# Kernel optimization log

Hardware: AMD Instinct MI355X
Metric: run time of the kernel (lower is better)

## Reference

```python
import jax, jax.numpy as jnp
import numpy as np

T, B, D = 160, 640, 40      # time-major frames, batch (N_spk*M_utt), log-mel dim
H, P, L = 768, 256, 3       # nb_hidden, nb_proj, nb_layers


def setup_inputs() -> dict:
    key = jax.random.key(0)
    ks = jax.random.split(key, 1 + 3 * L)
    inp = {"x": jax.random.normal(ks[0], (T, B, D), jnp.float32)}
    din = D
    for l in range(L):
        gs = np.float32(np.sqrt(2.0 / (din + P + 4 * H)))  # glorot-ish scale
        inp[f"W{l}"] = jax.random.normal(ks[1 + 3 * l], (din + P, 4 * H), jnp.float32) * gs
        inp[f"b{l}"] = jnp.zeros((4 * H,), jnp.float32)
        ps = np.float32(np.sqrt(2.0 / (H + P)))
        inp[f"Wp{l}"] = jax.random.normal(ks[3 + 3 * l], (H, P), jnp.float32) * ps
        din = P
    return inp


def lstmp_layer(x, W, b, Wp):
    # x: [T, B, d_in] time-major. TF LSTMCell with num_proj: state h has dim P,
    # gate order (i, j, f, o), forget_bias = 1.0.
    bsz = x.shape[1]
    c0 = jnp.zeros((bsz, H), x.dtype)
    h0 = jnp.zeros((bsz, P), x.dtype)

    def step(carry, xt):
        c, h = carry
        z = jnp.concatenate([xt, h], axis=-1) @ W + b            # [B, 4H]
        i, j, f, o = jnp.split(z, 4, axis=-1)
        c = jax.nn.sigmoid(f + 1.0) * c + jax.nn.sigmoid(i) * jnp.tanh(j)
        h = (jax.nn.sigmoid(o) * jnp.tanh(c)) @ Wp               # projection -> [B, P]
        return (c, h), h

    _, ys = jax.lax.scan(step, (c0, h0), x)                      # ys: [T, B, P]
    return ys


def reference(x, W0, b0, Wp0, W1, b1, Wp1, W2, b2, Wp2):
    h = lstmp_layer(x, W0, b0, Wp0)
    h = lstmp_layer(h, W1, b1, Wp1)
    h = lstmp_layer(h, W2, b2, Wp2)
    emb = h[-1]                                                  # last timestep: [B, P]
    return emb / (jnp.linalg.norm(emb, axis=-1, keepdims=True) + 1e-6)
```

## Files before the change

### kernel.cpp

```cpp
#include <hip/hip_runtime.h>
#include <hip/hip_bf16.h>

typedef __attribute__((ext_vector_type(4))) float f32x4;
typedef __attribute__((ext_vector_type(8))) short s16x8;

#define DEVFN static __device__ __forceinline__

#define TT  160
#define BB  640
#define DD  40
#define HH  768
#define PP  256
#define G4H 3072

#define NWG   192
#define NTHR  256

#define KH  256
#define KX0 64

#define STW1 328
#define STW2 520
#define STP  776
#define LDS_ELEMS 66560

#define XP_BYTES   (TT*BB*64*2)
#define HR_BYTES   (3*4*BB*PP*2)
#define SB_BYTES   (3*BB*HH*2)
#define XP_OFF     0
#define HR_OFF     (XP_OFF + XP_BYTES)
#define SB_OFF     (HR_OFF + HR_BYTES)
#define SYNC_OFF   (SB_OFF + SB_BYTES)
#define SYNC_BYTES 4096

DEVFN float sigm(float v)  { return __fdividef(1.f, 1.f + __expf(-v)); }
DEVFN float tanh_(float v) { return 2.f * __fdividef(1.f, 1.f + __expf(-2.f * v)) - 1.f; }
DEVFN f32x4 f4zero() { f32x4 v; v[0]=0.f; v[1]=0.f; v[2]=0.f; v[3]=0.f; return v; }

DEVFN void gst_b16(__hip_bfloat16* p, __hip_bfloat16 v) {
  unsigned short u = __builtin_bit_cast(unsigned short, v);
  asm volatile("global_store_short %0, %1, off sc0 sc1" :: "v"(p), "v"(u));
}

DEVFN unsigned ld_cc(const unsigned* p) {
  unsigned v;
  asm volatile("global_load_dword %0, %1, off sc0 sc1\n\ts_waitcnt vmcnt(0)"
               : "=v"(v) : "v"(p) : "memory");
  return v;
}
DEVFN void st_cc(unsigned* p, unsigned v) {
  asm volatile("global_store_dword %0, %1, off sc0 sc1" :: "v"(p), "v"(v) : "memory");
}
DEVFN void ld3_cc(const unsigned* p0, const unsigned* p1, const unsigned* p2,
                  unsigned& a, unsigned& b, unsigned& c) {
  asm volatile("global_load_dword %0, %3, off sc0 sc1\n\t"
               "global_load_dword %1, %4, off sc0 sc1\n\t"
               "global_load_dword %2, %5, off sc0 sc1\n\t"
               "s_waitcnt vmcnt(0)"
               : "=&v"(a), "=&v"(b), "=&v"(c)
               : "v"(p0), "v"(p1), "v"(p2) : "memory");
}

DEVFN void fence_acq() { __builtin_amdgcn_fence(__ATOMIC_ACQUIRE, "agent"); }

#define SFLAG(s,l,g) ((s) + 256 + ((l)*48+(g))*4)
#define PFLAG(s,l,p) ((s) + 832 + ((l)*16+(p))*4)

DEVFN void init_barrier(unsigned* sync, int bid, int tid) {
  __syncthreads();
  if (tid == 0) st_cc(sync + bid, 1u);
  if (tid < 64) {
    unsigned a, b, c;
    for (;;) {
      ld3_cc(sync + tid, sync + 64 + tid, sync + 128 + tid, a, b, c);
      if (__all((a >= 1u) & (b >= 1u) & (c >= 1u))) break;
    }
    fence_acq();
  }
  __syncthreads();
}

DEVFN void wait_flags(const unsigned* base, int nf, int thr, int tid) {
  if (thr <= 0) return;
  if (tid < 64) {
    const unsigned* p = base + tid * 4;
    for (;;) {
      int v = (tid < nf) ? (int)ld_cc(p) : 0x7fffffff;
      if (__all(v >= thr)) break;
    }
    fence_acq();
  }
  __syncthreads();
}

DEVFN void wait_proj(const unsigned* sf_l, const unsigned* sf_lp1, int has2,
                     int thr1, int thr2, int tid) {
  if (tid < 64) {
    const unsigned* p1 = sf_l + tid * 4;
    const unsigned* p2 = sf_lp1 + tid * 4;
    for (;;) {
      int v1 = (tid < 48) ? (int)ld_cc(p1) : 0x7fffffff;
      int v2 = (has2 && tid < 48 && thr2 > 0) ? (int)ld_cc(p2) : 0x7fffffff;
      if (__all((v1 >= thr1) & (v2 >= thr2))) break;
    }
    fence_acq();
  }
  __syncthreads();
}

DEVFN void set_flag(unsigned* p, unsigned v, int tid) {
  __syncthreads();
  if (tid == 0) st_cc(p, v);
}

__global__ __launch_bounds__(NTHR, 1)
void lstmp_persistent(const float* __restrict__ xin,
                      const float* __restrict__ W0, const float* __restrict__ b0, const float* __restrict__ Wp0,
                      const float* __restrict__ W1, const float* __restrict__ b1, const float* __restrict__ Wp1,
                      const float* __restrict__ W2, const float* __restrict__ b2, const float* __restrict__ Wp2,
                      float* __restrict__ outp, unsigned char* __restrict__ ws)
{
  __shared__ __align__(16) __hip_bfloat16 lds[LDS_ELEMS];

  const int bid  = blockIdx.x;
  const int tid  = threadIdx.x;
  const int lane = tid & 63;
  const int wave = tid >> 6;
  const int q    = lane >> 4;
  const int c16  = lane & 15;

  __hip_bfloat16* Xp = (__hip_bfloat16*)(ws + XP_OFF);
  __hip_bfloat16* Hr = (__hip_bfloat16*)(ws + HR_OFF);
  __hip_bfloat16* Sb = (__hip_bfloat16*)(ws + SB_OFF);
  unsigned* sync     = (unsigned*)(ws + SYNC_OFF);

  const int xcd  = bid & 7;
  const int slot = bid >> 3;
  const bool isGate = (xcd < 6);
  int l = 0, bc = 0, hg = 0, mt = 0, nt = 0;
  if (isGate) { l = xcd >> 1; bc = xcd & 1; hg = slot; }
  else        { l = slot >> 3; int r = slot & 7; mt = (xcd - 6) * 2 + (r >> 2); nt = r & 3; }

  const int KX  = (l == 0) ? KX0 : 256;
  const int KT  = KX + KH;
  const int STW = (l == 0) ? STW1 : STW2;

  const float* Wl  = (l == 0) ? W0  : ((l == 1) ? W1  : W2);
  const float* bl  = (l == 0) ? b0  : ((l == 1) ? b1  : b2);
  const float* Wpl = (l == 0) ? Wp0 : ((l == 1) ? Wp1 : Wp2);

  for (int e = bid * NTHR + tid; e < TT * BB * 64; e += NWG * NTHR) {
    int k  = e & 63;
    int tb = e >> 6;
    float v = (k < DD) ? xin[(size_t)tb * DD + k] : 0.f;
    gst_b16(&Xp[e], __float2bfloat16(v));
  }

  if (isGate) {
    for (int idx = tid; idx < 128 * KT; idx += NTHR) {
      int kk = idx >> 7;
      int nn = idx & 127;
      int col = (nn >> 5) * HH + hg * 32 + (nn & 31);
      float v;
      if (l == 0) {
        v = (kk < DD) ? Wl[(size_t)kk * G4H + col]
                      : ((kk < KX0) ? 0.f : Wl[(size_t)(kk - 24) * G4H + col]);
      } else {
        v = Wl[(size_t)kk * G4H + col];
      }
      lds[nn * STW + kk] = __float2bfloat16(v);
    }
  } else {
    for (int idx = tid; idx < 64 * HH; idx += NTHR) {
      int kk = idx >> 6;
      int nn = idx & 63;
      lds[nn * STP + kk] = __float2bfloat16(Wpl[(size_t)kk * PP + nt * 64 + nn]);
    }
  }

  init_barrier(sync, bid, tid);

  if (isGate) {
    const int gid = bc * 24 + hg;
    unsigned* myflag = SFLAG(sync, l, gid);
    const unsigned* pf_own = PFLAG(sync, l, 0);
    const unsigned* pf_prv = (l > 0) ? PFLAG(sync, l - 1, 0) : PFLAG(sync, l, 0);

    const int wmg = wave >> 1, wng = wave & 1;
    const int m0g = bc * 320 + wmg * 160;
    const int hcl = wng * 16 + c16;
    float biasv[4];
#pragma unroll
    for (int g = 0; g < 4; ++g) biasv[g] = bl[g * HH + hg * 32 + hcl];

    f32x4 acc[10][4];
    float cst[10][4];
#pragma unroll
    for (int mi = 0; mi < 10; ++mi)
#pragma unroll
      for (int g = 0; g < 4; ++g) { acc[mi][g] = f4zero(); cst[mi][g] = 0.f; }

    auto gate_gemm = [&](const __hip_bfloat16* A, int lda, int kbase, int klen) {
      s16x8 avA[5], avB[5];
#pragma unroll
      for (int mi = 0; mi < 5; ++mi)
        avA[mi] = *(const s16x8*)(A + (size_t)(m0g + mi * 16 + c16) * lda + 8 * q);
#pragma unroll 1
      for (int ks = 0; ks < klen; ks += 32) {
#pragma unroll
        for (int mi = 0; mi < 5; ++mi)
          avB[mi] = *(const s16x8*)(A + (size_t)(m0g + (5 + mi) * 16 + c16) * lda + ks + 8 * q);
        s16x8 bv[4];
#pragma unroll
        for (int g = 0; g < 4; ++g)
          bv[g] = *(const s16x8*)(lds + (g * 32 + hcl) * STW + kbase + ks + 8 * q);
#pragma unroll
        for (int mi = 0; mi < 5; ++mi)
#pragma unroll
          for (int g = 0; g < 4; ++g)
            acc[mi][g] = __builtin_amdgcn_mfma_f32_16x16x32_bf16(avA[mi], bv[g], acc[mi][g], 0, 0, 0);
        if (ks + 32 < klen) {
#pragma unroll
          for (int mi = 0; mi < 5; ++mi)
            avA[mi] = *(const s16x8*)(A + (size_t)(m0g + mi * 16 + c16) * lda + ks + 32 + 8 * q);
        }
#pragma unroll
        for (int mi = 0; mi < 5; ++mi)
#pragma unroll
          for (int g = 0; g < 4; ++g)
            acc[5 + mi][g] = __builtin_amdgcn_mfma_f32_16x16x32_bf16(avB[mi], bv[g], acc[5 + mi][g], 0, 0, 0);
      }
    };

    auto gate_update = [&]() {
      __hip_bfloat16* S = Sb + (size_t)l * BB * HH;
#pragma unroll
      for (int mi = 0; mi < 10; ++mi) {
#pragma unroll
        for (int r = 0; r < 4; ++r) {
          float iv = acc[mi][0][r] + biasv[0];
          float jv = acc[mi][1][r] + biasv[1];
          float fv = acc[mi][2][r] + biasv[2];
          float ov = acc[mi][3][r] + biasv[3];
          float c  = sigm(fv + 1.f) * cst[mi][r] + sigm(iv) * tanh_(jv);
          cst[mi][r] = c;
          float sv = sigm(ov) * tanh_(c);
          gst_b16(&S[(size_t)(m0g + mi * 16 + q * 4 + r) * HH + hg * 32 + hcl],
                  __float2bfloat16(sv));
        }
#pragma unroll
        for (int g = 0; g < 4; ++g) acc[mi][g] = f4zero();
      }
    };

    if (l == 0) gate_gemm(Xp, 64, 0, KX0);
    else {
      wait_flags(pf_prv, 16, 1, tid);
      gate_gemm(Hr + ((size_t)(l - 1) * 4 + 1) * BB * PP, PP, 0, 256);
    }

    for (int t = 0; t < TT; ++t) {
      wait_flags(pf_own, 16, t, tid);
      gate_gemm(Hr + ((size_t)l * 4 + ((unsigned)t & 3)) * BB * PP, PP, KX, KH);
      gate_update();
      set_flag(myflag, (unsigned)(t + 1), tid);
      if (t + 1 < TT) {
        if (l == 0) gate_gemm(Xp + (size_t)(t + 1) * BB * 64, 64, 0, KX0);
        else {
          wait_flags(pf_prv, 16, t + 2, tid);
          gate_gemm(Hr + ((size_t)(l - 1) * 4 + ((unsigned)(t + 2) & 3)) * BB * PP, PP, 0, 256);
        }
      }
    }
  } else {
    const int pid = mt * 4 + nt;
    unsigned* myflag = PFLAG(sync, l, pid);
    const unsigned* sf_own = SFLAG(sync, l, 0);
    const unsigned* sf_nxt = (l < 2) ? SFLAG(sync, l + 1, 0) : SFLAG(sync, l, 0);
    const int m0p = mt * 160 + (wave >> 1) * 80;
    const int np0 = (wave & 1) * 32;

    for (int t = 0; t < TT; ++t) {
      wait_proj(sf_own, sf_nxt, l < 2 ? 1 : 0, t + 1, t - 3, tid);

      const __hip_bfloat16* A = Sb + (size_t)l * BB * HH;
      const __hip_bfloat16* ab[5];
#pragma unroll
      for (int mi = 0; mi < 5; ++mi)
        ab[mi] = A + (size_t)(m0p + mi * 16 + c16) * HH + 8 * q;

      f32x4 pa[5][2];
#pragma unroll
      for (int mi = 0; mi < 5; ++mi) { pa[mi][0] = f4zero(); pa[mi][1] = f4zero(); }

      s16x8 a0[5], a1[5];
#pragma unroll
      for (int mi = 0; mi < 5; ++mi) a0[mi] = *(const s16x8*)(ab[mi] + 0);

#pragma unroll 1
      for (int it2 = 0; it2 < 12; ++it2) {
        const int ks0 = it2 * 64, ks1 = ks0 + 32;
#pragma unroll
        for (int mi = 0; mi < 5; ++mi) a1[mi] = *(const s16x8*)(ab[mi] + ks1);
        s16x8 bv[2];
#pragma unroll
        for (int ni = 0; ni < 2; ++ni)
          bv[ni] = *(const s16x8*)(lds + (np0 + ni * 16 + c16) * STP + ks0 + 8 * q);
#pragma unroll
        for (int mi = 0; mi < 5; ++mi)
#pragma unroll
          for (int ni = 0; ni < 2; ++ni)
            pa[mi][ni] = __builtin_amdgcn_mfma_f32_16x16x32_bf16(a0[mi], bv[ni], pa[mi][ni], 0, 0, 0);
        if (it2 < 11) {
#pragma unroll
          for (int mi = 0; mi < 5; ++mi) a0[mi] = *(const s16x8*)(ab[mi] + ks0 + 64);
        }
#pragma unroll
        for (int ni = 0; ni < 2; ++ni)
          bv[ni] = *(const s16x8*)(lds + (np0 + ni * 16 + c16) * STP + ks1 + 8 * q);
#pragma unroll
        for (int mi = 0; mi < 5; ++mi)
#pragma unroll
          for (int ni = 0; ni < 2; ++ni)
            pa[mi][ni] = __builtin_amdgcn_mfma_f32_16x16x32_bf16(a1[mi], bv[ni], pa[mi][ni], 0, 0, 0);
      }

      __hip_bfloat16* Hd = Hr + ((size_t)l * 4 + ((unsigned)(t + 1) & 3)) * BB * PP;
#pragma unroll
      for (int mi = 0; mi < 5; ++mi)
#pragma unroll
        for (int ni = 0; ni < 2; ++ni)
#pragma unroll
          for (int r = 0; r < 4; ++r)
            gst_b16(&Hd[(size_t)(m0p + mi * 16 + q * 4 + r) * PP + nt * 64 + np0 + ni * 16 + c16],
                    __float2bfloat16(pa[mi][ni][r]));

      set_flag(myflag, (unsigned)(t + 1), tid);
    }
  }

  wait_flags(PFLAG(sync, 2, 0), 16, TT, tid);
  const __hip_bfloat16* hf = Hr + (size_t)(2 * 4 + 0) * BB * PP;
  float* red = reinterpret_cast<float*>(lds);
  for (int row = bid; row < BB; row += NWG) {
    float v = __bfloat162float(hf[(size_t)row * PP + tid]);
    float ssq = v * v;
#pragma unroll
    for (int off = 32; off > 0; off >>= 1) ssq += __shfl_down(ssq, off, 64);
    if (lane == 0) red[wave] = ssq;
    __syncthreads();
    float tot = red[0] + red[1] + red[2] + red[3];
    outp[(size_t)row * PP + tid] = v * __fdividef(1.f, sqrtf(tot) + 1e-6f);
    __syncthreads();
  }
}

extern "C" void kernel_launch(void* const* d_in, const int* in_sizes, int n_in,
                              void* d_out, int out_size, void* d_ws, size_t ws_size,
                              hipStream_t stream) {
  (void)in_sizes; (void)n_in; (void)out_size; (void)ws_size;
  unsigned char* ws = (unsigned char*)d_ws;
  hipMemsetAsync(ws + HR_OFF, 0, HR_BYTES, stream);
  hipMemsetAsync(ws + SYNC_OFF, 0, SYNC_BYTES, stream);
  lstmp_persistent<<<dim3(NWG), dim3(NTHR), 0, stream>>>(
      (const float*)d_in[0],
      (const float*)d_in[1], (const float*)d_in[2], (const float*)d_in[3],
      (const float*)d_in[4], (const float*)d_in[5], (const float*)d_in[6],
      (const float*)d_in[7], (const float*)d_in[8], (const float*)d_in[9],
      (float*)d_out, ws);
}
```

Baseline: 5.608 ms.

## Narrow flag waits to per-batch-chunk producers and deepen projection GEMM prefetch

```diff
diff --git a/kernel.cpp b/kernel.cpp
--- a/kernel.cpp
+++ b/kernel.cpp
@@ -99,8 +99,8 @@
     const unsigned* p1 = sf_l + tid * 4;
     const unsigned* p2 = sf_lp1 + tid * 4;
     for (;;) {
-      int v1 = (tid < 48) ? (int)ld_cc(p1) : 0x7fffffff;
-      int v2 = (has2 && tid < 48 && thr2 > 0) ? (int)ld_cc(p2) : 0x7fffffff;
+      int v1 = (tid < 24) ? (int)ld_cc(p1) : 0x7fffffff;
+      int v2 = (has2 && tid < 24 && thr2 > 0) ? (int)ld_cc(p2) : 0x7fffffff;
       if (__all((v1 >= thr1) & (v2 >= thr2))) break;
     }
     fence_acq();
@@ -183,8 +183,8 @@
   if (isGate) {
     const int gid = bc * 24 + hg;
     unsigned* myflag = SFLAG(sync, l, gid);
-    const unsigned* pf_own = PFLAG(sync, l, 0);
-    const unsigned* pf_prv = (l > 0) ? PFLAG(sync, l - 1, 0) : PFLAG(sync, l, 0);
+    const unsigned* pf_own = PFLAG(sync, l, bc * 8);
+    const unsigned* pf_prv = (l > 0) ? PFLAG(sync, l - 1, bc * 8) : PFLAG(sync, l, bc * 8);
 
     const int wmg = wave >> 1, wng = wave & 1;
     const int m0g = bc * 320 + wmg * 160;
@@ -255,28 +255,29 @@
 
     if (l == 0) gate_gemm(Xp, 64, 0, KX0);
     else {
-      wait_flags(pf_prv, 16, 1, tid);
+      wait_flags(pf_prv, 8, 1, tid);
       gate_gemm(Hr + ((size_t)(l - 1) * 4 + 1) * BB * PP, PP, 0, 256);
     }
 
     for (int t = 0; t < TT; ++t) {
-      wait_flags(pf_own, 16, t, tid);
+      wait_flags(pf_own, 8, t, tid);
       gate_gemm(Hr + ((size_t)l * 4 + ((unsigned)t & 3)) * BB * PP, PP, KX, KH);
       gate_update();
       set_flag(myflag, (unsigned)(t + 1), tid);
       if (t + 1 < TT) {
         if (l == 0) gate_gemm(Xp + (size_t)(t + 1) * BB * 64, 64, 0, KX0);
         else {
-          wait_flags(pf_prv, 16, t + 2, tid);
+          wait_flags(pf_prv, 8, t + 2, tid);
           gate_gemm(Hr + ((size_t)(l - 1) * 4 + ((unsigned)(t + 2) & 3)) * BB * PP, PP, 0, 256);
         }
       }
     }
   } else {
     const int pid = mt * 4 + nt;
+    const int bch = mt >> 1;
     unsigned* myflag = PFLAG(sync, l, pid);
-    const unsigned* sf_own = SFLAG(sync, l, 0);
-    const unsigned* sf_nxt = (l < 2) ? SFLAG(sync, l + 1, 0) : SFLAG(sync, l, 0);
+    const unsigned* sf_own = SFLAG(sync, l, bch * 24);
+    const unsigned* sf_nxt = (l < 2) ? SFLAG(sync, l + 1, bch * 24) : SFLAG(sync, l, bch * 24);
     const int m0p = mt * 160 + (wave >> 1) * 80;
     const int np0 = (wave & 1) * 32;
 
@@ -293,37 +294,38 @@
 #pragma unroll
       for (int mi = 0; mi < 5; ++mi) { pa[mi][0] = f4zero(); pa[mi][1] = f4zero(); }
 
-      s16x8 a0[5], a1[5];
-#pragma unroll
-      for (int mi = 0; mi < 5; ++mi) a0[mi] = *(const s16x8*)(ab[mi] + 0);
-
-#pragma unroll 1
-      for (int it2 = 0; it2 < 12; ++it2) {
-        const int ks0 = it2 * 64, ks1 = ks0 + 32;
-#pragma unroll
-        for (int mi = 0; mi < 5; ++mi) a1[mi] = *(const s16x8*)(ab[mi] + ks1);
-        s16x8 bv[2];
-#pragma unroll
-        for (int ni = 0; ni < 2; ++ni)
-          bv[ni] = *(const s16x8*)(lds + (np0 + ni * 16 + c16) * STP + ks0 + 8 * q);
-#pragma unroll
-        for (int mi = 0; mi < 5; ++mi)
-#pragma unroll
-          for (int ni = 0; ni < 2; ++ni)
-            pa[mi][ni] = __builtin_amdgcn_mfma_f32_16x16x32_bf16(a0[mi], bv[ni], pa[mi][ni], 0, 0, 0);
-        if (it2 < 11) {
-#pragma unroll
-          for (int mi = 0; mi < 5; ++mi) a0[mi] = *(const s16x8*)(ab[mi] + ks0 + 64);
-        }
-#pragma unroll
-        for (int ni = 0; ni < 2; ++ni)
-          bv[ni] = *(const s16x8*)(lds + (np0 + ni * 16 + c16) * STP + ks1 + 8 * q);
-#pragma unroll
-        for (int mi = 0; mi < 5; ++mi)
-#pragma unroll
-          for (int ni = 0; ni < 2; ++ni)
-            pa[mi][ni] = __builtin_amdgcn_mfma_f32_16x16x32_bf16(a1[mi], bv[ni], pa[mi][ni], 0, 0, 0);
-      }
+      s16x8 r0[5], r1[5], r2[5], r3[5];
+#pragma unroll
+      for (int mi = 0; mi < 5; ++mi) {
+        r0[mi] = *(const s16x8*)(ab[mi] + 0);
+        r1[mi] = *(const s16x8*)(ab[mi] + 32);
+        r2[mi] = *(const s16x8*)(ab[mi] + 64);
+        r3[mi] = *(const s16x8*)(ab[mi] + 96);
+      }
+
+#define PSLICE(RB, S)                                                          \
+      {                                                                        \
+        s16x8 bv0 = *(const s16x8*)(lds + (np0 + c16) * STP + (S) * 32 + 8 * q);      \
+        s16x8 bv1 = *(const s16x8*)(lds + (np0 + 16 + c16) * STP + (S) * 32 + 8 * q); \
+        _Pragma("unroll")                                                      \
+        for (int mi = 0; mi < 5; ++mi) {                                       \
+          pa[mi][0] = __builtin_amdgcn_mfma_f32_16x16x32_bf16(RB[mi], bv0, pa[mi][0], 0, 0, 0); \
+          pa[mi][1] = __builtin_amdgcn_mfma_f32_16x16x32_bf16(RB[mi], bv1, pa[mi][1], 0, 0, 0); \
+        }                                                                      \
+        if ((S) + 4 < 24) {                                                    \
+          _Pragma("unroll")                                                    \
+          for (int mi = 0; mi < 5; ++mi)                                       \
+            RB[mi] = *(const s16x8*)(ab[mi] + ((S) + 4) * 32);                 \
+        }                                                                      \
+      }
+
+      PSLICE(r0, 0)  PSLICE(r1, 1)  PSLICE(r2, 2)  PSLICE(r3, 3)
+      PSLICE(r0, 4)  PSLICE(r1, 5)  PSLICE(r2, 6)  PSLICE(r3, 7)
+      PSLICE(r0, 8)  PSLICE(r1, 9)  PSLICE(r2, 10) PSLICE(r3, 11)
+      PSLICE(r0, 12) PSLICE(r1, 13) PSLICE(r2, 14) PSLICE(r3, 15)
+      PSLICE(r0, 16) PSLICE(r1, 17) PSLICE(r2, 18) PSLICE(r3, 19)
+      PSLICE(r0, 20) PSLICE(r1, 21) PSLICE(r2, 22) PSLICE(r3, 23)
+#undef PSLICE
 
       __hip_bfloat16* Hd = Hr + ((size_t)l * 4 + ((unsigned)(t + 1) & 3)) * BB * PP;
 #pragma unroll
```

After: 5.611 ms. No clear change (+0.1%).
